# Performance work log

Measured on AMD Instinct MI355X. Metric: run time of the kernel, lower is better.

## Reference

```python
import jax, jax.numpy as jnp
import numpy as np

N_NODES = 200000
IN_FEAT = 500
EMB = 128
HID = 64
N_CLASSES = 7


def setup_inputs() -> dict:
    key = jax.random.key(0)
    ks = jax.random.split(key, 7)
    scale = 0.05
    return {
        "adj": jnp.zeros((N_NODES,), dtype=jnp.float32),  # unused in pretrain path
        "features": jax.random.normal(ks[0], (N_NODES, IN_FEAT), dtype=jnp.float32),
        "W_emb": jax.random.normal(ks[1], (IN_FEAT, EMB), dtype=jnp.float32) * scale,
        "b_emb": jax.random.normal(ks[2], (EMB,), dtype=jnp.float32) * scale,
        "W_rt1": jax.random.normal(ks[3], (EMB, HID), dtype=jnp.float32) * scale,
        "b_rt1": jax.random.normal(ks[4], (HID,), dtype=jnp.float32) * scale,
        "W_rt2": jax.random.normal(ks[5], (HID, N_CLASSES), dtype=jnp.float32) * scale,
        "b_rt2": jax.random.normal(ks[6], (N_CLASSES,), dtype=jnp.float32) * scale,
    }


def reference(adj, features, W_emb, b_emb, W_rt1, b_rt1, W_rt2, b_rt2):
    # Policy.forward with pretrain=True:
    #   feature = ReLU(features @ W_emb + b_emb)        (get_embedding)
    #   res = (ReLU(feature @ W_rt1 + b_rt1)) @ W_rt2 + b_rt2   (get_rt, act='relu')
    emb = jax.nn.relu(features @ W_emb + b_emb)      # [N, EMB]
    h = jax.nn.relu(emb @ W_rt1 + b_rt1)             # [N, HID]
    return h @ W_rt2 + b_rt2                         # [N, N_CLASSES]
```

## Files before the change

### kernel.cpp

```cpp
#include <hip/hip_runtime.h>
#include <hip/hip_bf16.h>

typedef unsigned short u16;
typedef __bf16 bf16x8 __attribute__((ext_vector_type(8)));
typedef float f32x4 __attribute__((ext_vector_type(4)));

#define N_NODES 200000
#define IN_FEAT 500
#define EMB 128
#define HID 64
#define NC 7
#define BM 64
#define KPAD 512

#define FS 40
#define WS 40
#define W1S 136
#define ES 136
#define HS 72
#define W2S 72

#define WS_WT1_OFF (128*512)
#define WS_WT2_OFF (128*512 + 64*128)
#define WS_TOTAL   (128*512 + 64*128 + 16*64)

__device__ __forceinline__ u16 cvt_bf16(float v) {
    __hip_bfloat16 h = __float2bfloat16(v);
    return *(u16*)&h;
}

__global__ __launch_bounds__(256) void prep_weights(
    const float* __restrict__ W_emb, const float* __restrict__ W_rt1,
    const float* __restrict__ W_rt2, u16* __restrict__ ws)
{
    int idx = blockIdx.x * 256 + threadIdx.x;
    float v;
    bool ok = true;
    if (idx < 128*512) {
        int n = idx >> 9, k = idx & 511;
        v = (k < IN_FEAT) ? W_emb[k*EMB + n] : 0.f;
    } else if (idx < WS_WT2_OFF) {
        int j = idx - WS_WT1_OFF;
        int n = j >> 7, k = j & 127;
        v = W_rt1[k*HID + n];
    } else if (idx < WS_TOTAL) {
        int j = idx - WS_WT2_OFF;
        int n = j >> 6, k = j & 63;
        v = (n < NC) ? W_rt2[k*NC + n] : 0.f;
    } else {
        ok = false;
        v = 0.f;
    }
    if (ok) ws[idx] = cvt_bf16(v);
}

__global__ __launch_bounds__(256) void mlp_fused(
    const float* __restrict__ F, const u16* __restrict__ Wt_emb,
    const u16* __restrict__ Wt1g, const u16* __restrict__ Wt2g,
    const float* __restrict__ b_emb, const float* __restrict__ b1,
    const float* __restrict__ b2, float* __restrict__ out)
{
    __shared__ u16 Fch[BM * FS];
    __shared__ u16 Wch[EMB * WS];
    __shared__ u16 W1l[HID * W1S];
    __shared__ u16 W2l[16 * W2S];
    __shared__ u16 Et[BM * ES];
    __shared__ u16 Ht[BM * HS];

    const int tid  = threadIdx.x;
    const int wave = tid >> 6;
    const int lane = tid & 63;
    const int l15  = lane & 15;
    const int q    = lane >> 4;
    const int row0 = blockIdx.x * BM;

    #pragma unroll
    for (int i = 0; i < 4; ++i) {
        int g = tid * 4 + i;
        int r = g >> 4, cc = (g & 15) * 8;
        *(uint4*)&W1l[r*W1S + cc] = *(const uint4*)&Wt1g[r*128 + cc];
    }
    if (tid < 128) {
        int r = tid >> 3, cc = (tid & 7) * 8;
        *(uint4*)&W2l[r*W2S + cc] = *(const uint4*)&Wt2g[r*64 + cc];
    }

    f32x4 acc[8];
    #pragma unroll
    for (int t = 0; t < 8; ++t) acc[t] = (f32x4){0.f,0.f,0.f,0.f};

    for (int c = 0; c < 16; ++c) {
        const int k0 = c * 32;
        {
            int r = tid >> 2, g = tid & 3;
            const float* src = F + (size_t)(row0 + r) * IN_FEAT + k0 + g * 8;
            union { u16 u[8]; uint4 v4; } pk;
            if (c < 15 || g < 2) {
                float4 f0 = *(const float4*)(src);
                float4 f1 = *(const float4*)(src + 4);
                pk.u[0] = cvt_bf16(f0.x); pk.u[1] = cvt_bf16(f0.y);
                pk.u[2] = cvt_bf16(f0.z); pk.u[3] = cvt_bf16(f0.w);
                pk.u[4] = cvt_bf16(f1.x); pk.u[5] = cvt_bf16(f1.y);
                pk.u[6] = cvt_bf16(f1.z); pk.u[7] = cvt_bf16(f1.w);
            } else {
                #pragma unroll
                for (int j = 0; j < 8; ++j) {
                    int k = k0 + g * 8 + j;
                    pk.u[j] = (k < IN_FEAT) ? cvt_bf16(src[j]) : (u16)0;
                }
            }
            *(uint4*)&Fch[r*FS + g*8] = pk.v4;
        }
        {
            int n = tid >> 1, h = (tid & 1) * 16;
            *(uint4*)&Wch[n*WS + h]     = *(const uint4*)&Wt_emb[n*KPAD + k0 + h];
            *(uint4*)&Wch[n*WS + h + 8] = *(const uint4*)&Wt_emb[n*KPAD + k0 + h + 8];
        }
        __syncthreads();

        bf16x8 a = *(const bf16x8*)&Fch[(wave*16 + l15)*FS + q*8];
        #pragma unroll
        for (int t = 0; t < 8; ++t) {
            bf16x8 b = *(const bf16x8*)&Wch[(t*16 + l15)*WS + q*8];
            acc[t] = __builtin_amdgcn_mfma_f32_16x16x32_bf16(a, b, acc[t], 0, 0, 0);
        }
        __syncthreads();
    }

    #pragma unroll
    for (int t = 0; t < 8; ++t) {
        float bias = b_emb[t*16 + l15];
        #pragma unroll
        for (int r = 0; r < 4; ++r) {
            float v = acc[t][r] + bias;
            v = v > 0.f ? v : 0.f;
            Et[(wave*16 + q*4 + r)*ES + t*16 + l15] = cvt_bf16(v);
        }
    }
    __syncthreads();

    f32x4 acc2[4];
    #pragma unroll
    for (int t = 0; t < 4; ++t) acc2[t] = (f32x4){0.f,0.f,0.f,0.f};
    #pragma unroll
    for (int kc = 0; kc < 4; ++kc) {
        bf16x8 a = *(const bf16x8*)&Et[(wave*16 + l15)*ES + kc*32 + q*8];
        #pragma unroll
        for (int t = 0; t < 4; ++t) {
            bf16x8 b = *(const bf16x8*)&W1l[(t*16 + l15)*W1S + kc*32 + q*8];
            acc2[t] = __builtin_amdgcn_mfma_f32_16x16x32_bf16(a, b, acc2[t], 0, 0, 0);
        }
    }
    #pragma unroll
    for (int t = 0; t < 4; ++t) {
        float bias = b1[t*16 + l15];
        #pragma unroll
        for (int r = 0; r < 4; ++r) {
            float v = acc2[t][r] + bias;
            v = v > 0.f ? v : 0.f;
            Ht[(wave*16 + q*4 + r)*HS + t*16 + l15] = cvt_bf16(v);
        }
    }
    __syncthreads();

    f32x4 acc3 = (f32x4){0.f,0.f,0.f,0.f};
    #pragma unroll
    for (int kc = 0; kc < 2; ++kc) {
        bf16x8 a = *(const bf16x8*)&Ht[(wave*16 + l15)*HS + kc*32 + q*8];
        bf16x8 b = *(const bf16x8*)&W2l[l15*W2S + kc*32 + q*8];
        acc3 = __builtin_amdgcn_mfma_f32_16x16x32_bf16(a, b, acc3, 0, 0, 0);
    }
    if (l15 < NC) {
        float bias = b2[l15];
        #pragma unroll
        for (int r = 0; r < 4; ++r) {
            float v = acc3[r] + bias;
            out[(size_t)(row0 + wave*16 + q*4 + r) * NC + l15] = v;
        }
    }
}

extern "C" void kernel_launch(void* const* d_in, const int* in_sizes, int n_in,
                              void* d_out, int out_size, void* d_ws, size_t ws_size,
                              hipStream_t stream) {
    const float* F     = (const float*)d_in[1];
    const float* W_emb = (const float*)d_in[2];
    const float* b_emb = (const float*)d_in[3];
    const float* W_rt1 = (const float*)d_in[4];
    const float* b_rt1 = (const float*)d_in[5];
    const float* W_rt2 = (const float*)d_in[6];
    const float* b_rt2 = (const float*)d_in[7];
    u16* ws    = (u16*)d_ws;
    float* out = (float*)d_out;

    int prep_blocks = (WS_TOTAL + 255) / 256;
    prep_weights<<<prep_blocks, 256, 0, stream>>>(W_emb, W_rt1, W_rt2, ws);

    mlp_fused<<<N_NODES / BM, 256, 0, stream>>>(
        F, ws, ws + WS_WT1_OFF, ws + WS_WT2_OFF,
        b_emb, b_rt1, b_rt2, out);
}
```

Baseline: 593.9 us.

## Prefetch feature tiles into registers and read weights directly from global

Raises the K chunk from 32 to 64 and software-pipelines the feature load: the next chunk's fp32 values are fetched into registers while the current bf16 tile in shared memory feeds the MFMAs. Embedding, rt1 and rt2 weights are no longer staged in LDS and are instead loaded straight from global memory (L1/L2-cached) per MFMA. This drops one barrier per iteration and cuts LDS use, and a launch-bounds occupancy hint of 4 blocks is added. The cost is more global and cache traffic for weight fragments and higher register pressure.

Measured after the change: 691.2 us. +16.4%, slower.

```diff
diff --git a/kernel.cpp b/kernel.cpp
--- a/kernel.cpp
+++ b/kernel.cpp
@@ -11,14 +11,12 @@
 #define HID 64
 #define NC 7
 #define BM 64
+#define BK 64
 #define KPAD 512
 
-#define FS 40
-#define WS 40
-#define W1S 136
+#define FS 72
 #define ES 136
 #define HS 72
-#define W2S 72
 
 #define WS_WT1_OFF (128*512)
 #define WS_WT2_OFF (128*512 + 64*128)
@@ -47,23 +45,17 @@
         int j = idx - WS_WT2_OFF;
         int n = j >> 6, k = j & 63;
         v = (n < NC) ? W_rt2[k*NC + n] : 0.f;
-    } else {
-        ok = false;
-        v = 0.f;
-    }
+    } else { ok = false; v = 0.f; }
     if (ok) ws[idx] = cvt_bf16(v);
 }
 
-__global__ __launch_bounds__(256) void mlp_fused(
+__global__ __launch_bounds__(256, 4) void mlp_fused(
     const float* __restrict__ F, const u16* __restrict__ Wt_emb,
     const u16* __restrict__ Wt1g, const u16* __restrict__ Wt2g,
     const float* __restrict__ b_emb, const float* __restrict__ b1,
     const float* __restrict__ b2, float* __restrict__ out)
 {
     __shared__ u16 Fch[BM * FS];
-    __shared__ u16 Wch[EMB * WS];
-    __shared__ u16 W1l[HID * W1S];
-    __shared__ u16 W2l[16 * W2S];
     __shared__ u16 Et[BM * ES];
     __shared__ u16 Ht[BM * HS];
 
@@ -74,67 +66,66 @@
     const int q    = lane >> 4;
     const int row0 = blockIdx.x * BM;
 
-    #pragma unroll
-    for (int i = 0; i < 4; ++i) {
-        int g = tid * 4 + i;
-        int r = g >> 4, cc = (g & 15) * 8;
-        *(uint4*)&W1l[r*W1S + cc] = *(const uint4*)&Wt1g[r*128 + cc];
-    }
-    if (tid < 128) {
-        int r = tid >> 3, cc = (tid & 7) * 8;
-        *(uint4*)&W2l[r*W2S + cc] = *(const uint4*)&Wt2g[r*64 + cc];
-    }
+    const int r = tid >> 2, g = tid & 3;
+    const float* Frow = F + (size_t)(row0 + r) * IN_FEAT + g * 16;
 
     f32x4 acc[8];
     #pragma unroll
     for (int t = 0; t < 8; ++t) acc[t] = (f32x4){0.f,0.f,0.f,0.f};
 
-    for (int c = 0; c < 16; ++c) {
-        const int k0 = c * 32;
-        {
-            int r = tid >> 2, g = tid & 3;
-            const float* src = F + (size_t)(row0 + r) * IN_FEAT + k0 + g * 8;
-            union { u16 u[8]; uint4 v4; } pk;
-            if (c < 15 || g < 2) {
-                float4 f0 = *(const float4*)(src);
-                float4 f1 = *(const float4*)(src + 4);
-                pk.u[0] = cvt_bf16(f0.x); pk.u[1] = cvt_bf16(f0.y);
-                pk.u[2] = cvt_bf16(f0.z); pk.u[3] = cvt_bf16(f0.w);
-                pk.u[4] = cvt_bf16(f1.x); pk.u[5] = cvt_bf16(f1.y);
-                pk.u[6] = cvt_bf16(f1.z); pk.u[7] = cvt_bf16(f1.w);
-            } else {
-                #pragma unroll
-                for (int j = 0; j < 8; ++j) {
-                    int k = k0 + g * 8 + j;
-                    pk.u[j] = (k < IN_FEAT) ? cvt_bf16(src[j]) : (u16)0;
-                }
-            }
-            *(uint4*)&Fch[r*FS + g*8] = pk.v4;
-        }
-        {
-            int n = tid >> 1, h = (tid & 1) * 16;
-            *(uint4*)&Wch[n*WS + h]     = *(const uint4*)&Wt_emb[n*KPAD + k0 + h];
-            *(uint4*)&Wch[n*WS + h + 8] = *(const uint4*)&Wt_emb[n*KPAD + k0 + h + 8];
-        }
+    float4 pf0, pf1, pf2, pf3;
+    pf0 = *(const float4*)(Frow + 0);
+    pf1 = *(const float4*)(Frow + 4);
+    pf2 = *(const float4*)(Frow + 8);
+    pf3 = *(const float4*)(Frow + 12);
+
+    for (int c = 0; c < 8; ++c) {
+        union { u16 u[16]; uint4 v4[2]; } pk;
+        pk.u[0]=cvt_bf16(pf0.x); pk.u[1]=cvt_bf16(pf0.y); pk.u[2]=cvt_bf16(pf0.z); pk.u[3]=cvt_bf16(pf0.w);
+        pk.u[4]=cvt_bf16(pf1.x); pk.u[5]=cvt_bf16(pf1.y); pk.u[6]=cvt_bf16(pf1.z); pk.u[7]=cvt_bf16(pf1.w);
+        pk.u[8]=cvt_bf16(pf2.x); pk.u[9]=cvt_bf16(pf2.y); pk.u[10]=cvt_bf16(pf2.z); pk.u[11]=cvt_bf16(pf2.w);
+        pk.u[12]=cvt_bf16(pf3.x); pk.u[13]=cvt_bf16(pf3.y); pk.u[14]=cvt_bf16(pf3.z); pk.u[15]=cvt_bf16(pf3.w);
+        if (c > 0) __syncthreads();
+        *(uint4*)&Fch[r*FS + g*16]     = pk.v4[0];
+        *(uint4*)&Fch[r*FS + g*16 + 8] = pk.v4[1];
         __syncthreads();
 
-        bf16x8 a = *(const bf16x8*)&Fch[(wave*16 + l15)*FS + q*8];
+        if (c < 7) {
+            const float* src = Frow + (c + 1) * BK;
+            if (c < 6) {
+                pf0 = *(const float4*)(src + 0);
+                pf1 = *(const float4*)(src + 4);
+                pf2 = *(const float4*)(src + 8);
+                pf3 = *(const float4*)(src + 12);
+            } else {
+                pf0 = *(const float4*)(src + 0);
+                pf1 = (g < 3) ? *(const float4*)(src + 4)  : make_float4(0,0,0,0);
+                pf2 = (g < 3) ? *(const float4*)(src + 8)  : make_float4(0,0,0,0);
+                pf3 = (g < 3) ? *(const float4*)(src + 12) : make_float4(0,0,0,0);
+            }
+        }
+
         #pragma unroll
-        for (int t = 0; t < 8; ++t) {
-            bf16x8 b = *(const bf16x8*)&Wch[(t*16 + l15)*WS + q*8];
-            acc[t] = __builtin_amdgcn_mfma_f32_16x16x32_bf16(a, b, acc[t], 0, 0, 0);
+        for (int sub = 0; sub < 2; ++sub) {
+            bf16x8 a = *(const bf16x8*)&Fch[(wave*16 + l15)*FS + sub*32 + q*8];
+            const u16* wb = Wt_emb + l15*KPAD + c*BK + sub*32 + q*8;
+            #pragma unroll
+            for (int t = 0; t < 8; ++t) {
+                bf16x8 b = *(const bf16x8*)(wb + t*16*KPAD);
+                acc[t] = __builtin_amdgcn_mfma_f32_16x16x32_bf16(a, b, acc[t], 0, 0, 0);
+            }
         }
-        __syncthreads();
     }
+    __syncthreads();
 
     #pragma unroll
     for (int t = 0; t < 8; ++t) {
         float bias = b_emb[t*16 + l15];
         #pragma unroll
-        for (int r = 0; r < 4; ++r) {
-            float v = acc[t][r] + bias;
+        for (int rr = 0; rr < 4; ++rr) {
+            float v = acc[t][rr] + bias;
             v = v > 0.f ? v : 0.f;
-            Et[(wave*16 + q*4 + r)*ES + t*16 + l15] = cvt_bf16(v);
+            Et[(wave*16 + q*4 + rr)*ES + t*16 + l15] = cvt_bf16(v);
         }
     }
     __syncthreads();
@@ -147,7 +138,7 @@
         bf16x8 a = *(const bf16x8*)&Et[(wave*16 + l15)*ES + kc*32 + q*8];
         #pragma unroll
         for (int t = 0; t < 4; ++t) {
-            bf16x8 b = *(const bf16x8*)&W1l[(t*16 + l15)*W1S + kc*32 + q*8];
+            bf16x8 b = *(const bf16x8*)&Wt1g[(t*16 + l15)*128 + kc*32 + q*8];
             acc2[t] = __builtin_amdgcn_mfma_f32_16x16x32_bf16(a, b, acc2[t], 0, 0, 0);
         }
     }
@@ -155,10 +146,10 @@
     for (int t = 0; t < 4; ++t) {
         float bias = b1[t*16 + l15];
         #pragma unroll
-        for (int r = 0; r < 4; ++r) {
-            float v = acc2[t][r] + bias;
+        for (int rr = 0; rr < 4; ++rr) {
+            float v = acc2[t][rr] + bias;
             v = v > 0.f ? v : 0.f;
-            Ht[(wave*16 + q*4 + r)*HS + t*16 + l15] = cvt_bf16(v);
+            Ht[(wave*16 + q*4 + rr)*HS + t*16 + l15] = cvt_bf16(v);
         }
     }
     __syncthreads();
@@ -167,15 +158,14 @@
     #pragma unroll
     for (int kc = 0; kc < 2; ++kc) {
         bf16x8 a = *(const bf16x8*)&Ht[(wave*16 + l15)*HS + kc*32 + q*8];
-        bf16x8 b = *(const bf16x8*)&W2l[l15*W2S + kc*32 + q*8];
+        bf16x8 b = *(const bf16x8*)&Wt2g[l15*64 + kc*32 + q*8];
         acc3 = __builtin_amdgcn_mfma_f32_16x16x32_bf16(a, b, acc3, 0, 0, 0);
     }
     if (l15 < NC) {
         float bias = b2[l15];
         #pragma unroll
-        for (int r = 0; r < 4; ++r) {
-            float v = acc3[r] + bias;
-            out[(size_t)(row0 + wave*16 + q*4 + r) * NC + l15] = v;
+        for (int rr = 0; rr < 4; ++rr) {
+            out[(size_t)(row0 + wave*16 + q*4 + rr) * NC + l15] = acc3[rr] + bias;
         }
     }
 }
```
